# Kernel tuning notes

Hardware: AMD Instinct MI355X
Metric: run time of the kernel (lower is better)

The kernel has to match this reference:

```python
import jax, jax.numpy as jnp
import numpy as np

N_NODES = 50000
N_EDGES = 800000
N_FEAT = 128
HIDDEN = 128
N_CLASSES = 10
N_LAYERS = 3
N_GRAPHS = 512


def setup_inputs() -> dict:
    key = jax.random.key(0)
    ks = jax.random.split(key, 16)
    s = 1.0 / np.sqrt(HIDDEN)
    inp = {
        "x": jax.random.normal(ks[0], (N_NODES, N_FEAT), jnp.float32),
        "edge_index": jax.random.randint(ks[1], (2, N_EDGES), 0, N_NODES, jnp.int64),
        "batch": jnp.sort(jax.random.randint(ks[2], (N_NODES,), 0, N_GRAPHS, jnp.int64)),
        "num_graphs": N_GRAPHS,
        "conv1_wl": jax.random.normal(ks[3], (N_FEAT, HIDDEN), jnp.float32) * s,
        "conv1_wr": jax.random.normal(ks[4], (N_FEAT, HIDDEN), jnp.float32) * s,
        "conv1_b": jnp.zeros((HIDDEN,), jnp.float32),
        "convs_wl": jax.random.normal(ks[5], (N_LAYERS - 1, HIDDEN, HIDDEN), jnp.float32) * s,
        "convs_wr": jax.random.normal(ks[6], (N_LAYERS - 1, HIDDEN, HIDDEN), jnp.float32) * s,
        "convs_b": jnp.zeros((N_LAYERS - 1, HIDDEN), jnp.float32),
        "gate_w": jax.random.normal(ks[7], (HIDDEN, 1), jnp.float32) * s,
        "gate_b": jnp.zeros((1,), jnp.float32),
        "lin1_w": jax.random.normal(ks[8], (HIDDEN, HIDDEN), jnp.float32) * s,
        "lin1_b": jnp.zeros((HIDDEN,), jnp.float32),
        "lin2_w": jax.random.normal(ks[9], (HIDDEN, N_CLASSES), jnp.float32) * s,
        "lin2_b": jnp.zeros((N_CLASSES,), jnp.float32),
    }
    return inp


def _sage_conv(x, src, dst, inv_deg, wl, wr, b):
    # mean aggregation of source-node features at destination nodes
    agg = jax.ops.segment_sum(x[src], dst, num_segments=N_NODES)  # [N, d]
    agg = agg * inv_deg
    return agg @ wl + x @ wr + b


def _global_attention(x, batch, num_graphs, gate_w, gate_b):
    gate = (x @ gate_w + gate_b)[:, 0]                      # [N]
    m = jax.ops.segment_max(gate, batch, num_segments=num_graphs)
    m = jnp.where(jnp.isfinite(m), m, 0.0)
    g = jnp.exp(gate - m[batch])                            # stable segment softmax
    den = jax.ops.segment_sum(g, batch, num_segments=num_graphs)
    attn = g / den[batch]
    return jax.ops.segment_sum(attn[:, None] * x, batch, num_segments=num_graphs)


def reference(x, edge_index, batch, num_graphs,
              conv1_wl, conv1_wr, conv1_b,
              convs_wl, convs_wr, convs_b,
              gate_w, gate_b, lin1_w, lin1_b, lin2_w, lin2_b):
    src, dst = edge_index[0], edge_index[1]
    deg = jax.ops.segment_sum(jnp.ones((src.shape[0],), x.dtype), dst,
                              num_segments=N_NODES)
    inv_deg = (1.0 / jnp.maximum(deg, 1.0))[:, None]

    h = jax.nn.relu(_sage_conv(x, src, dst, inv_deg, conv1_wl, conv1_wr, conv1_b))
    for i in range(convs_wl.shape[0]):
        h = jax.nn.relu(_sage_conv(h, src, dst, inv_deg,
                                   convs_wl[i], convs_wr[i], convs_b[i]))

    pooled = _global_attention(h, batch, num_graphs, gate_w, gate_b)  # [G, H]
    out = jax.nn.relu(pooled @ lin1_w + lin1_b)
    # dropout p=0.5 is identity at eval time
    logits = out @ lin2_w + lin2_b
    return jax.nn.log_softmax(logits, axis=-1)
```

## Files before the change

kernel.cpp:

```cpp
#include <hip/hip_runtime.h>
#include <math.h>

#define N_NODES 50000
#define N_PAD   50048
#define N_EDGES 800000
#define FEAT 128
#define K2 256
#define N_GRAPHS 512
#define N_CLASSES 10
#define BCAP 64
#define RANGE_SZ 12500
#define BROW 264
#define OROW 72

typedef __attribute__((ext_vector_type(8))) short short8;
typedef __attribute__((ext_vector_type(4))) float floatx4;

__device__ __forceinline__ float bflo(unsigned u) { return __uint_as_float(u << 16); }
__device__ __forceinline__ float bfhi(unsigned u) { return __uint_as_float(u & 0xffff0000u); }
__device__ __forceinline__ unsigned short f2bf(float f) {
    unsigned u = __float_as_uint(f);
    u = (u + 0x7fffu + ((u >> 16) & 1u)) >> 16;
    return (unsigned short)u;
}
__device__ __forceinline__ unsigned pack2(float a, float b) {
    return (unsigned)f2bf(a) | ((unsigned)f2bf(b) << 16);
}

__global__ __launch_bounds__(256) void fill_bucket(
    const int* __restrict__ src, const int* __restrict__ dst,
    int* __restrict__ cnt, unsigned short* __restrict__ bucket) {
    int range = blockIdx.x & 3;
    int chunk = blockIdx.x >> 2;
    int e = chunk * 256 + threadIdx.x;
    int lo = range * RANGE_SZ;
    int d = dst[e];
    if (d >= lo && d < lo + RANGE_SZ) {
        int p = atomicAdd(&cnt[d], 1);
        if (p < BCAP) bucket[(size_t)d * BCAP + p] = (unsigned short)src[e];
    }
}

__global__ __launch_bounds__(256) void setup_kernel(
    const float* __restrict__ x, unsigned short* __restrict__ A,
    const float* __restrict__ wl1, const float* __restrict__ wr1,
    const float* __restrict__ wl23, const float* __restrict__ wr23,
    unsigned short* __restrict__ wt,
    const int* __restrict__ batch, int* __restrict__ goffs) {
    int b = blockIdx.x;
    if (b < 6250) {
        int idx = b * 256 + threadIdx.x;
        if (idx < N_NODES * 32) {
            int n = idx >> 5, f4 = idx & 31;
            float4 v = ((const float4*)(x + (size_t)n * FEAT))[f4];
            uint2 o = make_uint2(pack2(v.x, v.y), pack2(v.z, v.w));
            *(uint2*)(A + (size_t)n * K2 + FEAT + f4 * 4) = o;
        }
    } else if (b < 6250 + 384) {
        int idx = (b - 6250) * 256 + threadIdx.x;
        int layer = idx >> 15;
        int r = idx & 32767;
        int n = r >> 8, k = r & 255;
        const float* wl = (layer == 0) ? wl1 : wl23 + (size_t)(layer - 1) * FEAT * FEAT;
        const float* wr = (layer == 0) ? wr1 : wr23 + (size_t)(layer - 1) * FEAT * FEAT;
        float v = (k < FEAT) ? wl[k * FEAT + n] : wr[(k - FEAT) * FEAT + n];
        wt[idx] = f2bf(v);
    } else {
        int g = (b - 6250 - 384) * 256 + threadIdx.x;
        if (g > N_GRAPHS) return;
        int lo = 0, hi = N_NODES;
        while (lo < hi) {
            int mid = (lo + hi) >> 1;
            if (batch[mid] < g) lo = mid + 1; else hi = mid;
        }
        goffs[g] = lo;
    }
}

__device__ __forceinline__ void acc8(float* acc, uint4 u) {
    acc[0] += bflo(u.x); acc[1] += bfhi(u.x);
    acc[2] += bflo(u.y); acc[3] += bfhi(u.y);
    acc[4] += bflo(u.z); acc[5] += bfhi(u.z);
    acc[6] += bflo(u.w); acc[7] += bfhi(u.w);
}

__global__ __launch_bounds__(256) void aggregate_bf16(
    const unsigned short* __restrict__ hin, const int* __restrict__ cnt,
    const unsigned short* __restrict__ bucket, unsigned short* __restrict__ aggout) {
    int n = blockIdx.x * 4 + (threadIdx.x >> 6);
    if (n >= N_NODES) return;
    int lane = threadIdx.x & 63;
    int g = lane >> 4;
    int l16 = lane & 15;
    int deg = cnt[n];
    int c = min(deg, BCAP);
    int nq = c >> 2;
    int rem = c & 3;
    const unsigned short* cp = bucket + (size_t)n * BCAP;

    float acc[8];
    #pragma unroll
    for (int i = 0; i < 8; ++i) acc[i] = 0.f;

    int i = 0;
    for (; i + 4 <= nq; i += 4) {
        int s0 = cp[i * 4 + g];
        int s1 = cp[i * 4 + 4 + g];
        int s2 = cp[i * 4 + 8 + g];
        int s3 = cp[i * 4 + 12 + g];
        uint4 u0 = *(const uint4*)(hin + (size_t)s0 * K2 + l16 * 8);
        uint4 u1 = *(const uint4*)(hin + (size_t)s1 * K2 + l16 * 8);
        uint4 u2 = *(const uint4*)(hin + (size_t)s2 * K2 + l16 * 8);
        uint4 u3 = *(const uint4*)(hin + (size_t)s3 * K2 + l16 * 8);
        acc8(acc, u0); acc8(acc, u1); acc8(acc, u2); acc8(acc, u3);
    }
    if (i + 2 <= nq) {
        int s0 = cp[i * 4 + g];
        int s1 = cp[i * 4 + 4 + g];
        uint4 u0 = *(const uint4*)(hin + (size_t)s0 * K2 + l16 * 8);
        uint4 u1 = *(const uint4*)(hin + (size_t)s1 * K2 + l16 * 8);
        acc8(acc, u0); acc8(acc, u1);
        i += 2;
    }
    if (i < nq) {
        int s0 = cp[i * 4 + g];
        uint4 u0 = *(const uint4*)(hin + (size_t)s0 * K2 + l16 * 8);
        acc8(acc, u0);
    }
    if (g < rem) {
        int s0 = cp[nq * 4 + g];
        uint4 u0 = *(const uint4*)(hin + (size_t)s0 * K2 + l16 * 8);
        acc8(acc, u0);
    }
    #pragma unroll
    for (int j = 0; j < 8; ++j) {
        acc[j] += __shfl_xor(acc[j], 16);
        acc[j] += __shfl_xor(acc[j], 32);
    }
    if (g == 0) {
        float inv = 1.0f / fmaxf((float)deg, 1.0f);
        uint4 o;
        o.x = pack2(acc[0] * inv, acc[1] * inv);
        o.y = pack2(acc[2] * inv, acc[3] * inv);
        o.z = pack2(acc[4] * inv, acc[5] * inv);
        o.w = pack2(acc[6] * inv, acc[7] * inv);
        *(uint4*)(aggout + (size_t)n * K2 + l16 * 8) = o;
    }
}

__global__ __launch_bounds__(256) void gemm_mfma(
    const unsigned short* __restrict__ Ain, unsigned short* __restrict__ Aout,
    const unsigned short* __restrict__ Wt, const float* __restrict__ bias,
    const float* __restrict__ gate_w, float* __restrict__ gate) {
    __shared__ unsigned short sB[64 * BROW];
    __shared__ unsigned short sOut[4][32 * OROW];
    int t = threadIdx.x;
    int wave = t >> 6, lane = t & 63;
    int q = lane >> 4, l16 = lane & 15;
    int tileM = blockIdx.x >> 1;
    int nh = blockIdx.x & 1;
    int row0 = tileM * 128 + wave * 32;

    const unsigned short* pa0 = Ain + (size_t)(row0 + l16) * K2 + q * 8;
    const unsigned short* pa1 = pa0 + 16 * K2;
    short8 a0[8], a1[8];
    #pragma unroll
    for (int ks = 0; ks < 8; ++ks) {
        a0[ks] = *(const short8*)(pa0 + ks * 32);
        a1[ks] = *(const short8*)(pa1 + ks * 32);
    }

    #pragma unroll
    for (int i = 0; i < 8; ++i) {
        int flat = i * 256 + t;
        int rw = flat >> 5, fr = flat & 31;
        uint4 v = *((const uint4*)(Wt + (size_t)(nh * 64 + rw) * K2) + fr);
        *(uint4*)(&sB[rw * BROW + fr * 8]) = v;
    }
    __syncthreads();

    floatx4 acc[2][4];
    #pragma unroll
    for (int i = 0; i < 2; ++i)
        #pragma unroll
        for (int j = 0; j < 4; ++j) acc[i][j] = (floatx4){0.f, 0.f, 0.f, 0.f};

    #pragma unroll
    for (int ks = 0; ks < 8; ++ks) {
        #pragma unroll
        for (int nb = 0; nb < 4; ++nb) {
            short8 b = *(const short8*)(&sB[(nb * 16 + l16) * BROW + ks * 32 + q * 8]);
            acc[0][nb] = __builtin_amdgcn_mfma_f32_16x16x32_bf16(a0[ks], b, acc[0][nb], 0, 0, 0);
            acc[1][nb] = __builtin_amdgcn_mfma_f32_16x16x32_bf16(a1[ks], b, acc[1][nb], 0, 0, 0);
        }
    }

    float bv[4], gwv[4];
    #pragma unroll
    for (int nb = 0; nb < 4; ++nb) bv[nb] = bias[nh * 64 + nb * 16 + l16];
    if (gate_w) {
        #pragma unroll
        for (int nb = 0; nb < 4; ++nb) gwv[nb] = gate_w[nh * 64 + nb * 16 + l16];
    }

    #pragma unroll
    for (int band = 0; band < 2; ++band) {
        #pragma unroll
        for (int r = 0; r < 4; ++r) {
            int lr = band * 16 + q * 4 + r;
            float gsum = 0.f;
            #pragma unroll
            for (int nb = 0; nb < 4; ++nb) {
                float v = fmaxf(acc[band][nb][r] + bv[nb], 0.f);
                sOut[wave][lr * OROW + nb * 16 + l16] = f2bf(v);
                if (gate_w) gsum += v * gwv[nb];
            }
            if (gate_w) {
                gsum += __shfl_xor(gsum, 1);
                gsum += __shfl_xor(gsum, 2);
                gsum += __shfl_xor(gsum, 4);
                gsum += __shfl_xor(gsum, 8);
                int m = row0 + lr;
                if (l16 == 0 && m < N_NODES) atomicAdd(&gate[m], gsum);
            }
        }
    }

    int r2 = lane >> 1, h2 = lane & 1;
    size_t gbase = (size_t)(row0 + r2) * K2 + FEAT + nh * 64 + h2 * 32;
    #pragma unroll
    for (int j = 0; j < 2; ++j) {
        uint4 v0 = *(uint4*)(&sOut[wave][r2 * OROW + h2 * 32 + j * 16]);
        uint4 v1 = *(uint4*)(&sOut[wave][r2 * OROW + h2 * 32 + j * 16 + 8]);
        *(uint4*)(Aout + gbase + j * 16) = v0;
        *(uint4*)(Aout + gbase + j * 16 + 8) = v1;
    }
}

__global__ __launch_bounds__(256) void pool_head(
    const unsigned short* __restrict__ h, const float* __restrict__ gate,
    const int* __restrict__ goffs,
    const float* __restrict__ w1, const float* __restrict__ b1,
    const float* __restrict__ w2, const float* __restrict__ b2,
    float* __restrict__ out) {
    __shared__ float sred[4];
    __shared__ float facc[4][128];
    __shared__ float pv[128], qv[128], lg[N_CLASSES];
    int g = blockIdx.x;
    int s = goffs[g], e = goffs[g + 1];
    int t = threadIdx.x;
    int wave = t >> 6, lane = t & 63;

    if (s < e) {
        float mx = -INFINITY;
        for (int n = s + t; n < e; n += 256) mx = fmaxf(mx, gate[n]);
        #pragma unroll
        for (int off = 32; off; off >>= 1) mx = fmaxf(mx, __shfl_xor(mx, off));
        if (lane == 0) sred[wave] = mx;
        __syncthreads();
        float m = fmaxf(fmaxf(sred[0], sred[1]), fmaxf(sred[2], sred[3]));
        __syncthreads();
        float d = 0.f;
        for (int n = s + t; n < e; n += 256) d += __expf(gate[n] - m);
        #pragma unroll
        for (int off = 32; off; off >>= 1) d += __shfl_xor(d, off);
        if (lane == 0) sred[wave] = d;
        __syncthreads();
        float den = sred[0] + sred[1] + sred[2] + sred[3];
        float acc0 = 0.f, acc1 = 0.f;
        for (int n = s + wave; n < e; n += 4) {
            float gn = __expf(gate[n] - m);
            unsigned u = *(const unsigned*)(h + (size_t)n * K2 + lane * 2);
            acc0 += gn * bflo(u);
            acc1 += gn * bfhi(u);
        }
        facc[wave][lane * 2]     = acc0;
        facc[wave][lane * 2 + 1] = acc1;
        __syncthreads();
        if (t < 128) pv[t] = (facc[0][t] + facc[1][t] + facc[2][t] + facc[3][t]) / den;
    } else {
        if (t < 128) pv[t] = 0.f;
    }
    __syncthreads();

    if (t < 128) {
        float acc = b1[t];
        #pragma unroll 4
        for (int k = 0; k < 128; ++k) acc += pv[k] * w1[k * FEAT + t];
        qv[t] = fmaxf(acc, 0.f);
    }
    __syncthreads();
    if (t < N_CLASSES) {
        float a = b2[t];
        #pragma unroll 4
        for (int k = 0; k < 128; ++k) a += qv[k] * w2[k * N_CLASSES + t];
        lg[t] = a;
    }
    __syncthreads();
    if (t < N_CLASSES) {
        float m = -INFINITY;
        #pragma unroll
        for (int j = 0; j < N_CLASSES; ++j) m = fmaxf(m, lg[j]);
        float sum = 0.f;
        #pragma unroll
        for (int j = 0; j < N_CLASSES; ++j) sum += __expf(lg[j] - m);
        out[(size_t)g * N_CLASSES + t] = lg[t] - m - __logf(sum);
    }
}

static inline size_t align256(size_t x) { return (x + 255) & ~(size_t)255; }

extern "C" void kernel_launch(void* const* d_in, const int* in_sizes, int n_in,
                              void* d_out, int out_size, void* d_ws, size_t ws_size,
                              hipStream_t stream) {
    const float* x        = (const float*)d_in[0];
    const int*   ei       = (const int*)d_in[1];
    const int*   batch    = (const int*)d_in[2];
    const float* conv1_wl = (const float*)d_in[4];
    const float* conv1_wr = (const float*)d_in[5];
    const float* conv1_b  = (const float*)d_in[6];
    const float* convs_wl = (const float*)d_in[7];
    const float* convs_wr = (const float*)d_in[8];
    const float* convs_b  = (const float*)d_in[9];
    const float* gate_w   = (const float*)d_in[10];
    const float* lin1_w   = (const float*)d_in[12];
    const float* lin1_b   = (const float*)d_in[13];
    const float* lin2_w   = (const float*)d_in[14];
    const float* lin2_b   = (const float*)d_in[15];
    float* out = (float*)d_out;

    const int* src = ei;
    const int* dst = ei + N_EDGES;

    char* w = (char*)d_ws;
    size_t off = 0;
    unsigned short* A0   = (unsigned short*)(w + off); off += align256((size_t)N_PAD * K2 * 2);
    unsigned short* A1   = (unsigned short*)(w + off); off += align256((size_t)N_PAD * K2 * 2);
    unsigned short* bkt  = (unsigned short*)(w + off); off += align256((size_t)N_NODES * BCAP * 2);
    unsigned short* wt   = (unsigned short*)(w + off); off += align256((size_t)3 * FEAT * K2 * 2);
    int*   i_goff = (int*)(w + off);   off += align256((size_t)(N_GRAPHS + 1) * 4);
    char* zbase = w + off;
    int*   i_cnt  = (int*)(w + off);   off += align256((size_t)N_NODES * 4);
    float* f_gate = (float*)(w + off); off += align256((size_t)N_NODES * 4);
    size_t zbytes = (size_t)((w + off) - zbase);

    hipMemsetAsync(zbase, 0, zbytes, stream);

    fill_bucket<<<12500, 256, 0, stream>>>(src, dst, i_cnt, bkt);
    setup_kernel<<<6250 + 384 + 3, 256, 0, stream>>>(
        x, A0, conv1_wl, conv1_wr, convs_wl, convs_wr, wt, batch, i_goff);

    const int AB = (N_NODES + 3) / 4;
    const int GB = (N_PAD / 128) * 2;

    aggregate_bf16<<<AB, 256, 0, stream>>>(A0 + FEAT, i_cnt, bkt, A0);
    gemm_mfma<<<GB, 256, 0, stream>>>(A0, A1, wt, conv1_b, nullptr, nullptr);
    aggregate_bf16<<<AB, 256, 0, stream>>>(A1 + FEAT, i_cnt, bkt, A1);
    gemm_mfma<<<GB, 256, 0, stream>>>(A1, A0, wt + FEAT * K2, convs_b, nullptr, nullptr);
    aggregate_bf16<<<AB, 256, 0, stream>>>(A0 + FEAT, i_cnt, bkt, A0);
    gemm_mfma<<<GB, 256, 0, stream>>>(A0, A1, wt + 2 * FEAT * K2, convs_b + FEAT,
                                      gate_w, f_gate);

    pool_head<<<N_GRAPHS, 256, 0, stream>>>(A1 + FEAT, f_gate, i_goff,
                                            lin1_w, lin1_b, lin2_w, lin2_b, out);
}
```

Baseline: 302.5 us.

## Use persistent aggregate with prefetch, XCD-aware GEMM remap, single-pass bucket fill

The aggregation kernel becomes a grid-stride persistent kernel over 2048 blocks. Each wave prefetches the next node's degree and bucket line while it aggregates the current node, to hide index-load latency. The GEMM remaps block IDs so that consecutive tiles land on the same XCD, which should improve L2 locality of the shared weight tiles. The bucket fill drops its four-pass dst range filter and processes every edge in one pass, trading more atomic contention for fewer redundant reads of dst.

```diff
diff --git a/kernel.cpp b/kernel.cpp
--- a/kernel.cpp
+++ b/kernel.cpp
@@ -9,9 +9,9 @@
 #define N_GRAPHS 512
 #define N_CLASSES 10
 #define BCAP 64
-#define RANGE_SZ 12500
 #define BROW 264
 #define OROW 72
+#define AGG_BLOCKS 2048
 
 typedef __attribute__((ext_vector_type(8))) short short8;
 typedef __attribute__((ext_vector_type(4))) float floatx4;
@@ -30,15 +30,10 @@
 __global__ __launch_bounds__(256) void fill_bucket(
     const int* __restrict__ src, const int* __restrict__ dst,
     int* __restrict__ cnt, unsigned short* __restrict__ bucket) {
-    int range = blockIdx.x & 3;
-    int chunk = blockIdx.x >> 2;
-    int e = chunk * 256 + threadIdx.x;
-    int lo = range * RANGE_SZ;
+    int e = blockIdx.x * 256 + threadIdx.x;
     int d = dst[e];
-    if (d >= lo && d < lo + RANGE_SZ) {
-        int p = atomicAdd(&cnt[d], 1);
-        if (p < BCAP) bucket[(size_t)d * BCAP + p] = (unsigned short)src[e];
-    }
+    int p = atomicAdd(&cnt[d], 1);
+    if (p < BCAP) bucket[(size_t)d * BCAP + p] = (unsigned short)src[e];
 }
 
 __global__ __launch_bounds__(256) void setup_kernel(
@@ -87,64 +82,81 @@
 __global__ __launch_bounds__(256) void aggregate_bf16(
     const unsigned short* __restrict__ hin, const int* __restrict__ cnt,
     const unsigned short* __restrict__ bucket, unsigned short* __restrict__ aggout) {
-    int n = blockIdx.x * 4 + (threadIdx.x >> 6);
-    if (n >= N_NODES) return;
     int lane = threadIdx.x & 63;
     int g = lane >> 4;
     int l16 = lane & 15;
+    int wid = (blockIdx.x << 2) + (threadIdx.x >> 6);
+    const int nw = gridDim.x << 2;
+
+    int n = wid;
+    if (n >= N_NODES) return;
     int deg = cnt[n];
-    int c = min(deg, BCAP);
-    int nq = c >> 2;
-    int rem = c & 3;
-    const unsigned short* cp = bucket + (size_t)n * BCAP;
-
-    float acc[8];
-    #pragma unroll
-    for (int i = 0; i < 8; ++i) acc[i] = 0.f;
-
-    int i = 0;
-    for (; i + 4 <= nq; i += 4) {
-        int s0 = cp[i * 4 + g];
-        int s1 = cp[i * 4 + 4 + g];
-        int s2 = cp[i * 4 + 8 + g];
-        int s3 = cp[i * 4 + 12 + g];
-        uint4 u0 = *(const uint4*)(hin + (size_t)s0 * K2 + l16 * 8);
-        uint4 u1 = *(const uint4*)(hin + (size_t)s1 * K2 + l16 * 8);
-        uint4 u2 = *(const uint4*)(hin + (size_t)s2 * K2 + l16 * 8);
-        uint4 u3 = *(const uint4*)(hin + (size_t)s3 * K2 + l16 * 8);
-        acc8(acc, u0); acc8(acc, u1); acc8(acc, u2); acc8(acc, u3);
-    }
-    if (i + 2 <= nq) {
-        int s0 = cp[i * 4 + g];
-        int s1 = cp[i * 4 + 4 + g];
-        uint4 u0 = *(const uint4*)(hin + (size_t)s0 * K2 + l16 * 8);
-        uint4 u1 = *(const uint4*)(hin + (size_t)s1 * K2 + l16 * 8);
-        acc8(acc, u0); acc8(acc, u1);
-        i += 2;
-    }
-    if (i < nq) {
-        int s0 = cp[i * 4 + g];
-        uint4 u0 = *(const uint4*)(hin + (size_t)s0 * K2 + l16 * 8);
-        acc8(acc, u0);
-    }
-    if (g < rem) {
-        int s0 = cp[nq * 4 + g];
-        uint4 u0 = *(const uint4*)(hin + (size_t)s0 * K2 + l16 * 8);
-        acc8(acc, u0);
-    }
-    #pragma unroll
-    for (int j = 0; j < 8; ++j) {
-        acc[j] += __shfl_xor(acc[j], 16);
-        acc[j] += __shfl_xor(acc[j], 32);
-    }
-    if (g == 0) {
-        float inv = 1.0f / fmaxf((float)deg, 1.0f);
-        uint4 o;
-        o.x = pack2(acc[0] * inv, acc[1] * inv);
-        o.y = pack2(acc[2] * inv, acc[3] * inv);
-        o.z = pack2(acc[4] * inv, acc[5] * inv);
-        o.w = pack2(acc[6] * inv, acc[7] * inv);
-        *(uint4*)(aggout + (size_t)n * K2 + l16 * 8) = o;
+
+    while (true) {
+        const unsigned short* cp = bucket + (size_t)n * BCAP;
+        int c = min(deg, BCAP);
+        int nq = c >> 2;
+        int rem = c & 3;
+
+        int nn = n + nw;
+        int dnext = 0;
+        if (nn < N_NODES) {
+            dnext = cnt[nn];
+            unsigned short bpre = bucket[(size_t)nn * BCAP + lane];
+            asm volatile("" :: "v"((int)bpre));
+        }
+
+        float acc[8];
+        #pragma unroll
+        for (int i = 0; i < 8; ++i) acc[i] = 0.f;
+
+        int i = 0;
+        for (; i + 4 <= nq; i += 4) {
+            int s0 = cp[i * 4 + g];
+            int s1 = cp[i * 4 + 4 + g];
+            int s2 = cp[i * 4 + 8 + g];
+            int s3 = cp[i * 4 + 12 + g];
+            uint4 u0 = *(const uint4*)(hin + (size_t)s0 * K2 + l16 * 8);
+            uint4 u1 = *(const uint4*)(hin + (size_t)s1 * K2 + l16 * 8);
+            uint4 u2 = *(const uint4*)(hin + (size_t)s2 * K2 + l16 * 8);
+            uint4 u3 = *(const uint4*)(hin + (size_t)s3 * K2 + l16 * 8);
+            acc8(acc, u0); acc8(acc, u1); acc8(acc, u2); acc8(acc, u3);
+        }
+        if (i + 2 <= nq) {
+            int s0 = cp[i * 4 + g];
+            int s1 = cp[i * 4 + 4 + g];
+            uint4 u0 = *(const uint4*)(hin + (size_t)s0 * K2 + l16 * 8);
+            uint4 u1 = *(const uint4*)(hin + (size_t)s1 * K2 + l16 * 8);
+            acc8(acc, u0); acc8(acc, u1);
+            i += 2;
+        }
+        if (i < nq) {
+            int s0 = cp[i * 4 + g];
+            uint4 u0 = *(const uint4*)(hin + (size_t)s0 * K2 + l16 * 8);
+            acc8(acc, u0);
+        }
+        if (g < rem) {
+            int s0 = cp[nq * 4 + g];
+            uint4 u0 = *(const uint4*)(hin + (size_t)s0 * K2 + l16 * 8);
+            acc8(acc, u0);
+        }
+        #pragma unroll
+        for (int j = 0; j < 8; ++j) {
+            acc[j] += __shfl_xor(acc[j], 16);
+            acc[j] += __shfl_xor(acc[j], 32);
+        }
+        if (g == 0) {
+            float inv = 1.0f / fmaxf((float)deg, 1.0f);
+            uint4 o;
+            o.x = pack2(acc[0] * inv, acc[1] * inv);
+            o.y = pack2(acc[2] * inv, acc[3] * inv);
+            o.z = pack2(acc[4] * inv, acc[5] * inv);
+            o.w = pack2(acc[6] * inv, acc[7] * inv);
+            *(uint4*)(aggout + (size_t)n * K2 + l16 * 8) = o;
+        }
+        if (nn >= N_NODES) break;
+        n = nn;
+        deg = dnext;
     }
 }
 
@@ -157,8 +169,14 @@
     int t = threadIdx.x;
     int wave = t >> 6, lane = t & 63;
     int q = lane >> 4, l16 = lane & 15;
-    int tileM = blockIdx.x >> 1;
-    int nh = blockIdx.x & 1;
+
+    const int nwg_q = 97, nwg_r = 6;
+    int orig = blockIdx.x;
+    int xcd = orig & 7, idx = orig >> 3;
+    int wgid = (xcd < nwg_r) ? xcd * (nwg_q + 1) + idx
+                             : nwg_r * (nwg_q + 1) + (xcd - nwg_r) * nwg_q + idx;
+    int tileM = wgid >> 1;
+    int nh = wgid & 1;
     int row0 = tileM * 128 + wave * 32;
 
     const unsigned short* pa0 = Ain + (size_t)(row0 + l16) * K2 + q * 8;
@@ -346,18 +364,17 @@
 
     hipMemsetAsync(zbase, 0, zbytes, stream);
 
-    fill_bucket<<<12500, 256, 0, stream>>>(src, dst, i_cnt, bkt);
+    fill_bucket<<<N_EDGES / 256, 256, 0, stream>>>(src, dst, i_cnt, bkt);
     setup_kernel<<<6250 + 384 + 3, 256, 0, stream>>>(
         x, A0, conv1_wl, conv1_wr, convs_wl, convs_wr, wt, batch, i_goff);
 
-    const int AB = (N_NODES + 3) / 4;
     const int GB = (N_PAD / 128) * 2;
 
-    aggregate_bf16<<<AB, 256, 0, stream>>>(A0 + FEAT, i_cnt, bkt, A0);
+    aggregate_bf16<<<AGG_BLOCKS, 256, 0, stream>>>(A0 + FEAT, i_cnt, bkt, A0);
     gemm_mfma<<<GB, 256, 0, stream>>>(A0, A1, wt, conv1_b, nullptr, nullptr);
-    aggregate_bf16<<<AB, 256, 0, stream>>>(A1 + FEAT, i_cnt, bkt, A1);
+    aggregate_bf16<<<AGG_BLOCKS, 256, 0, stream>>>(A1 + FEAT, i_cnt, bkt, A1);
     gemm_mfma<<<GB, 256, 0, stream>>>(A1, A0, wt + FEAT * K2, convs_b, nullptr, nullptr);
-    aggregate_bf16<<<AB, 256, 0, stream>>>(A0 + FEAT, i_cnt, bkt, A0);
+    aggregate_bf16<<<AGG_BLOCKS, 256, 0, stream>>>(A0 + FEAT, i_cnt, bkt, A0);
     gemm_mfma<<<GB, 256, 0, stream>>>(A0, A1, wt + 2 * FEAT * K2, convs_b + FEAT,
                                       gate_w, f_gate);
 
```

Result: no change. 305.2 us (+0.9%).
